# Optimization experiments

Measured on AMD Instinct MI355X. Metric: run time of the kernel, lower is better.

The kernel has to match this reference:

```python
import jax, jax.numpy as jnp
import numpy as np

K = 1024       # num_embeddings
D = 64         # embedding_dim
DECAY = 0.99
COMMIT = 0.25
EPS = 1e-05


def setup_inputs() -> dict:
    key = jax.random.key(0)
    k1, k2, k3 = jax.random.split(key, 3)
    x = jax.random.normal(k1, (16, 64, 64, 64), jnp.float32)  # NCHW, C == D
    embedding_weight = jax.random.normal(k2, (K, D), jnp.float32)
    ema_weight = jax.random.normal(k3, (K, D), jnp.float32)
    ema_cluster_size = jnp.zeros((K,), jnp.float32)
    return {"x": x, "embedding_weight": embedding_weight,
            "ema_cluster_size": ema_cluster_size, "ema_weight": ema_weight}


def reference(x, embedding_weight, ema_cluster_size, ema_weight):
    # NCHW -> NHWC, flatten tokens
    xp = jnp.transpose(x, (0, 2, 3, 1))            # [B,H,W,D]
    flat = xp.reshape(-1, D)                        # [N,D]
    dists = ((flat ** 2).sum(1, keepdims=True)
             + (embedding_weight ** 2).sum(1)
             - 2.0 * flat @ embedding_weight.T)     # [N,K]
    idx = jnp.argmin(dists, axis=1)                 # [N]
    encodings = jax.nn.one_hot(idx, K, dtype=flat.dtype)  # [N,K]
    quantized = jnp.take(embedding_weight, idx, axis=0).reshape(xp.shape)
    # training-mode EMA updates (scatter-add instead of dense one-hot matmuls)
    counts = jnp.zeros((K,), flat.dtype).at[idx].add(1.0)
    new_cs = ema_cluster_size * DECAY + (1.0 - DECAY) * counts
    n = new_cs.sum()
    new_cs = (new_cs + EPS) / (n + K * EPS) * n     # Laplace smoothing
    dw = jnp.zeros((K, D), flat.dtype).at[idx].add(flat)
    new_ema_weight = ema_weight * DECAY + (1.0 - DECAY) * dw
    new_embedding = new_ema_weight / new_cs[:, None]
    # commitment loss and straight-through estimator
    e_latent_loss = jnp.mean((jax.lax.stop_gradient(quantized) - xp) ** 2)
    loss = COMMIT * e_latent_loss
    q_st = xp + jax.lax.stop_gradient(quantized - xp)
    return (loss, jnp.transpose(q_st, (0, 3, 1, 2)), encodings,
            new_embedding, new_cs, new_ema_weight)
```

## Files before the change

kernel.cpp:

```cpp
#include <hip/hip_runtime.h>

#define HW 4096
#define DECAYF 0.99f
#define ONEMF 0.01f
#define EPSF 1e-5f

typedef __bf16 bf16x8 __attribute__((ext_vector_type(8)));
typedef float f32x4 __attribute__((ext_vector_type(4)));
typedef unsigned short ushort8 __attribute__((ext_vector_type(8)));

#define WS_COUNTS 65536
#define WS_NCHALF 66560
#define WS_SSE    67584
#define WS_EHI    67600
#define WS_ELO    100368

__device__ __forceinline__ float wave_reduce_add(float v) {
#pragma unroll
    for (int o = 32; o > 0; o >>= 1) v += __shfl_xor(v, o, 64);
    return v;
}

__device__ __forceinline__ unsigned short bf_rne(float f) {
    unsigned int u = __float_as_uint(f);
    unsigned int r = u + 0x7fffu + ((u >> 16) & 1u);
    return (unsigned short)(r >> 16);
}

__global__ __launch_bounds__(256) void prep_kernel(const float* __restrict__ E,
                                                   float* __restrict__ ws) {
    const int bid = blockIdx.x, tid = threadIdx.x;
    const int id = bid * 256 + tid;
    ws[id] = 0.0f;
    if (bid < 4) ws[WS_COUNTS + bid * 256 + tid] = 0.0f;
    if (bid == 4 && tid == 0) ws[WS_SSE] = 0.0f;
    const float v = E[id];
    const unsigned short h = bf_rne(v);
    const float hf = __uint_as_float((unsigned int)h << 16);
    const unsigned short l = bf_rne(v - hf);
    ((unsigned short*)(ws + WS_EHI))[id] = h;
    ((unsigned short*)(ws + WS_ELO))[id] = l;
    const int lane = tid & 63;
    const float s = wave_reduce_add(v * v);
    if (lane == 0) ws[WS_NCHALF + (id >> 6)] = -0.5f * s;
}

__global__ __launch_bounds__(256) void vq_main(const float* __restrict__ x,
                                               const float* __restrict__ E,
                                               float* __restrict__ out,
                                               float* __restrict__ ws) {
    const int tid = threadIdx.x;
    const int lane = tid & 63;
    const int w = tid >> 6;
    const int blk = blockIdx.x;
    const int b = blk >> 5;
    const int hw0 = (blk & 31) << 7;
    const int tok0 = blk << 7;

    __shared__ float xs[128 * 68];
    __shared__ int i1sh[128], i2sh[128], idx_sh[128];

    {
        const float* xb = x + ((size_t)b << 18) + hw0;
#pragma unroll
        for (int cc = 0; cc < 32; ++cc) {
            const int id = cc * 256 + tid;
            const int c = id >> 7, t = id & 127;
            xs[t * 68 + c] = xb[((size_t)c << 12) + t];
        }
    }
    __syncthreads();

    const int q = lane >> 4, m = lane & 15;

    bf16x8 Ah[2][2], Al[2][2];
#pragma unroll
    for (int t = 0; t < 2; ++t) {
        const int tok = w * 32 + t * 16 + m;
#pragma unroll
        for (int s = 0; s < 2; ++s) {
            const float* p = &xs[tok * 68 + s * 32 + q * 8];
            ushort8 hu, lu;
#pragma unroll
            for (int j = 0; j < 8; ++j) {
                const float f = p[j];
                const unsigned short h = bf_rne(f);
                const float hf = __uint_as_float((unsigned int)h << 16);
                hu[j] = h;
                lu[j] = bf_rne(f - hf);
            }
            Ah[t][s] = __builtin_bit_cast(bf16x8, hu);
            Al[t][s] = __builtin_bit_cast(bf16x8, lu);
        }
    }

    const ushort8* __restrict__ Ehp = (const ushort8*)(ws + WS_EHI);
    const ushort8* __restrict__ Elp = (const ushort8*)(ws + WS_ELO);
    const float* __restrict__ ncp = ws + WS_NCHALF;

    float b1[2][4], b2[2][4];
    int i1[2][4], i2[2][4];
#pragma unroll
    for (int t = 0; t < 2; ++t)
#pragma unroll
        for (int r = 0; r < 4; ++r) { b1[t][r] = -1e30f; b2[t][r] = -1e30f; i1[t][r] = 0; i2[t][r] = 1; }

    ushort8 nb0h = Ehp[m * 8 + q];
    ushort8 nb1h = Ehp[m * 8 + 4 + q];
    ushort8 nb0l = Elp[m * 8 + q];
    ushort8 nb1l = Elp[m * 8 + 4 + q];
    float nnc = ncp[m];

    for (int ck = 0; ck < 64; ++ck) {
        const ushort8 c0h = nb0h, c1h = nb1h, c0l = nb0l, c1l = nb1l;
        const float nc = nnc;
        if (ck < 63) {
            const int code = (ck + 1) * 16 + m;
            nb0h = Ehp[code * 8 + q];
            nb1h = Ehp[code * 8 + 4 + q];
            nb0l = Elp[code * 8 + q];
            nb1l = Elp[code * 8 + 4 + q];
            nnc = ncp[code];
        }
        const bf16x8 bh0 = __builtin_bit_cast(bf16x8, c0h);
        const bf16x8 bh1 = __builtin_bit_cast(bf16x8, c1h);
        const bf16x8 bl0 = __builtin_bit_cast(bf16x8, c0l);
        const bf16x8 bl1 = __builtin_bit_cast(bf16x8, c1l);
        const int idx = ck * 16 + m;
#pragma unroll
        for (int t = 0; t < 2; ++t) {
            f32x4 acc = {nc, nc, nc, nc};
            acc = __builtin_amdgcn_mfma_f32_16x16x32_bf16(Ah[t][0], bh0, acc, 0, 0, 0);
            acc = __builtin_amdgcn_mfma_f32_16x16x32_bf16(Ah[t][1], bh1, acc, 0, 0, 0);
            acc = __builtin_amdgcn_mfma_f32_16x16x32_bf16(Al[t][0], bh0, acc, 0, 0, 0);
            acc = __builtin_amdgcn_mfma_f32_16x16x32_bf16(Al[t][1], bh1, acc, 0, 0, 0);
            acc = __builtin_amdgcn_mfma_f32_16x16x32_bf16(Ah[t][0], bl0, acc, 0, 0, 0);
            acc = __builtin_amdgcn_mfma_f32_16x16x32_bf16(Ah[t][1], bl1, acc, 0, 0, 0);
#pragma unroll
            for (int r = 0; r < 4; ++r) {
                const float s = acc[r];
                const bool cA = s > b1[t][r];
                const bool cB = s > b2[t][r];
                b2[t][r] = cA ? b1[t][r] : (cB ? s : b2[t][r]);
                i2[t][r] = cA ? i1[t][r] : (cB ? idx : i2[t][r]);
                b1[t][r] = cA ? s : b1[t][r];
                i1[t][r] = cA ? idx : i1[t][r];
            }
        }
    }

#pragma unroll
    for (int d = 1; d < 16; d <<= 1) {
#pragma unroll
        for (int t = 0; t < 2; ++t)
#pragma unroll
            for (int r = 0; r < 4; ++r) {
                const float ob1 = __shfl_xor(b1[t][r], d, 64);
                const int   oi1 = __shfl_xor(i1[t][r], d, 64);
                const float ob2 = __shfl_xor(b2[t][r], d, 64);
                const int   oi2 = __shfl_xor(i2[t][r], d, 64);
                const bool wv = ob1 > b1[t][r];
                const float t1 = wv ? ob1 : b1[t][r]; const int ti1 = wv ? oi1 : i1[t][r];
                const float sA = wv ? b1[t][r] : ob1; const int siA = wv ? i1[t][r] : oi1;
                const float sB = wv ? ob2 : b2[t][r]; const int siB = wv ? oi2 : i2[t][r];
                const bool w2 = sB > sA;
                b1[t][r] = t1; i1[t][r] = ti1;
                b2[t][r] = w2 ? sB : sA; i2[t][r] = w2 ? siB : siA;
            }
    }
    if (m == 0) {
#pragma unroll
        for (int t = 0; t < 2; ++t)
#pragma unroll
            for (int r = 0; r < 4; ++r) {
                const int tokL = w * 32 + t * 16 + q * 4 + r;
                i1sh[tokL] = i1[t][r];
                i2sh[tokL] = i2[t][r];
            }
    }

    float dval = 0.0f;
    if (lane < 32) {
        const int tokL = w * 32 + lane;
        const int I1 = i1sh[tokL], I2 = i2sh[tokL];
        const int ca = I1 < I2 ? I1 : I2;
        const int cb = I1 < I2 ? I2 : I1;
        const float* Ea = E + ca * 64;
        const float* Eb = E + cb * 64;
        const float* xr = &xs[tokL * 68];
        double sa = 0, ea = 0, sb = 0, eb = 0, x2 = 0;
#pragma unroll 8
        for (int c = 0; c < 64; ++c) {
            const double xv = (double)xr[c];
            const double va = (double)Ea[c], vb = (double)Eb[c];
            sa += xv * va; ea += va * va;
            sb += xv * vb; eb += vb * vb;
            x2 += xv * xv;
        }
        const double qa = ea - 2.0 * sa;
        const double qb = eb - 2.0 * sb;
        int best; double qq;
        if (qb < qa) { best = cb; qq = qb; } else { best = ca; qq = qa; }
        idx_sh[tokL] = best;
        float dd = (float)(qq + x2);
        dval = dd < 0.f ? 0.f : dd;
        atomicAdd(&ws[WS_COUNTS + best], 1.0f);
    }
    const float ssum = wave_reduce_add(dval);
    if (lane == 0) atomicAdd(&ws[WS_SSE], ssum);
    __syncthreads();

    float* outq = out + 1;
#pragma unroll
    for (int cc = 0; cc < 32; ++cc) {
        const int id = cc * 256 + tid;
        const int c = id >> 7, t = id & 127;
        const int kb = idx_sh[t];
        const float xv = xs[t * 68 + c];
        const float eq = E[kb * 64 + c];
        outq[((size_t)(b * 64 + c) << 12) + hw0 + t] = xv + (eq - xv);
    }
#pragma unroll 4
    for (int tt = 0; tt < 32; ++tt) {
        const int t = w * 32 + tt;
        const int kb = idx_sh[t];
        atomicAdd(&ws[kb * 64 + lane], xs[t * 68 + lane]);
    }
    {
        float* enc = out + 1 + (size_t)4194304;
        const int c0 = tid << 2;
        for (int t = 0; t < 128; ++t) {
            const int kb = idx_sh[t];
            f32x4 v;
            v[0] = (c0 == kb) ? 1.0f : 0.0f;
            v[1] = (c0 + 1 == kb) ? 1.0f : 0.0f;
            v[2] = (c0 + 2 == kb) ? 1.0f : 0.0f;
            v[3] = (c0 + 3 == kb) ? 1.0f : 0.0f;
            __builtin_nontemporal_store(v, (f32x4*)(enc + (size_t)(tok0 + t) * 1024 + c0));
        }
    }
}

__global__ __launch_bounds__(1024) void fin_cs(const float* __restrict__ cs_in,
                                               float* __restrict__ out,
                                               const float* __restrict__ ws) {
    __shared__ float red[16];
    __shared__ float n_sh;
    const int tid = threadIdx.x;
    const float raw = cs_in[tid] * DECAYF + ONEMF * ws[WS_COUNTS + tid];
    const float s = wave_reduce_add(raw);
    if ((tid & 63) == 0) red[tid >> 6] = s;
    __syncthreads();
    if (tid == 0) {
        float n = 0.f;
#pragma unroll
        for (int i = 0; i < 16; ++i) n += red[i];
        n_sh = n;
        out[0] = 0.25f * ws[WS_SSE] * (1.0f / 4194304.0f);
    }
    __syncthreads();
    const float n = n_sh;
    out[71368705 + tid] = (raw + EPSF) / (n + 1024.0f * EPSF) * n;
}

__global__ __launch_bounds__(256) void fin_w(const float* __restrict__ emaw,
                                             float* __restrict__ out,
                                             const float* __restrict__ ws) {
    const int i = blockIdx.x * 256 + threadIdx.x;
    const float val = emaw[i] * DECAYF + ONEMF * ws[i];
    out[71369729 + i] = val;
    const float cs = out[71368705 + (i >> 6)];
    out[71303169 + i] = val / cs;
}

extern "C" void kernel_launch(void* const* d_in, const int* in_sizes, int n_in,
                              void* d_out, int out_size, void* d_ws, size_t ws_size,
                              hipStream_t stream) {
    const float* x    = (const float*)d_in[0];
    const float* E    = (const float*)d_in[1];
    const float* cs   = (const float*)d_in[2];
    const float* emaw = (const float*)d_in[3];
    float* out = (float*)d_out;
    float* ws  = (float*)d_ws;

    prep_kernel<<<256, 256, 0, stream>>>(E, ws);
    vq_main<<<512, 256, 0, stream>>>(x, E, out, ws);
    fin_cs<<<1, 1024, 0, stream>>>(cs, out, ws);
    fin_w<<<256, 256, 0, stream>>>(emaw, out, ws);
}
```

Baseline: 418.9 us.

## Split VQ kernel into scoring and output-writing kernels with double-buffered codebook prefetch

The fused kernel is split in two. vq_score computes the nearest-code indices and writes them to workspace. vq_out runs on 2048 blocks of 32 tokens and writes the quantized output, the one-hot encodings and the dw scatter-adds. The scoring loop now prefetches the codebook two steps ahead in alternating register slots instead of one. The aim is to spread the heavy encoding-write traffic (16M floats) over more blocks for better memory parallelism, and to hide codebook load latency. The cost is an extra launch, re-reading x, and an index round-trip through global memory.

```diff
diff --git a/kernel.cpp b/kernel.cpp
--- a/kernel.cpp
+++ b/kernel.cpp
@@ -1,6 +1,5 @@
 #include <hip/hip_runtime.h>
 
-#define HW 4096
 #define DECAYF 0.99f
 #define ONEMF 0.01f
 #define EPSF 1e-5f
@@ -14,6 +13,7 @@
 #define WS_SSE    67584
 #define WS_EHI    67600
 #define WS_ELO    100368
+#define WS_IDX    133136
 
 __device__ __forceinline__ float wave_reduce_add(float v) {
 #pragma unroll
@@ -45,10 +45,9 @@
     if (lane == 0) ws[WS_NCHALF + (id >> 6)] = -0.5f * s;
 }
 
-__global__ __launch_bounds__(256) void vq_main(const float* __restrict__ x,
-                                               const float* __restrict__ E,
-                                               float* __restrict__ out,
-                                               float* __restrict__ ws) {
+__global__ __launch_bounds__(256) void vq_score(const float* __restrict__ x,
+                                                const float* __restrict__ E,
+                                                float* __restrict__ ws) {
     const int tid = threadIdx.x;
     const int lane = tid & 63;
     const int w = tid >> 6;
@@ -58,7 +57,7 @@
     const int tok0 = blk << 7;
 
     __shared__ float xs[128 * 68];
-    __shared__ int i1sh[128], i2sh[128], idx_sh[128];
+    __shared__ int i1sh[128], i2sh[128];
 
     {
         const float* xb = x + ((size_t)b << 18) + hw0;
@@ -105,49 +104,61 @@
 #pragma unroll
         for (int r = 0; r < 4; ++r) { b1[t][r] = -1e30f; b2[t][r] = -1e30f; i1[t][r] = 0; i2[t][r] = 1; }
 
-    ushort8 nb0h = Ehp[m * 8 + q];
-    ushort8 nb1h = Ehp[m * 8 + 4 + q];
-    ushort8 nb0l = Elp[m * 8 + q];
-    ushort8 nb1l = Elp[m * 8 + 4 + q];
-    float nnc = ncp[m];
-
-    for (int ck = 0; ck < 64; ++ck) {
-        const ushort8 c0h = nb0h, c1h = nb1h, c0l = nb0l, c1l = nb1l;
-        const float nc = nnc;
-        if (ck < 63) {
-            const int code = (ck + 1) * 16 + m;
-            nb0h = Ehp[code * 8 + q];
-            nb1h = Ehp[code * 8 + 4 + q];
-            nb0l = Elp[code * 8 + q];
-            nb1l = Elp[code * 8 + 4 + q];
-            nnc = ncp[code];
-        }
-        const bf16x8 bh0 = __builtin_bit_cast(bf16x8, c0h);
-        const bf16x8 bh1 = __builtin_bit_cast(bf16x8, c1h);
-        const bf16x8 bl0 = __builtin_bit_cast(bf16x8, c0l);
-        const bf16x8 bl1 = __builtin_bit_cast(bf16x8, c1l);
-        const int idx = ck * 16 + m;
-#pragma unroll
-        for (int t = 0; t < 2; ++t) {
-            f32x4 acc = {nc, nc, nc, nc};
-            acc = __builtin_amdgcn_mfma_f32_16x16x32_bf16(Ah[t][0], bh0, acc, 0, 0, 0);
-            acc = __builtin_amdgcn_mfma_f32_16x16x32_bf16(Ah[t][1], bh1, acc, 0, 0, 0);
-            acc = __builtin_amdgcn_mfma_f32_16x16x32_bf16(Al[t][0], bh0, acc, 0, 0, 0);
-            acc = __builtin_amdgcn_mfma_f32_16x16x32_bf16(Al[t][1], bh1, acc, 0, 0, 0);
-            acc = __builtin_amdgcn_mfma_f32_16x16x32_bf16(Ah[t][0], bl0, acc, 0, 0, 0);
-            acc = __builtin_amdgcn_mfma_f32_16x16x32_bf16(Ah[t][1], bl1, acc, 0, 0, 0);
-#pragma unroll
-            for (int r = 0; r < 4; ++r) {
-                const float s = acc[r];
-                const bool cA = s > b1[t][r];
-                const bool cB = s > b2[t][r];
-                b2[t][r] = cA ? b1[t][r] : (cB ? s : b2[t][r]);
-                i2[t][r] = cA ? i1[t][r] : (cB ? idx : i2[t][r]);
-                b1[t][r] = cA ? s : b1[t][r];
-                i1[t][r] = cA ? idx : i1[t][r];
-            }
-        }
-    }
+    ushort8 p0h[2], p1h[2], p0l[2], p1l[2];
+    float pnc[2];
+#pragma unroll
+    for (int s = 0; s < 2; ++s) {
+        const int code = s * 16 + m;
+        p0h[s] = Ehp[code * 8 + q];
+        p1h[s] = Ehp[code * 8 + 4 + q];
+        p0l[s] = Elp[code * 8 + q];
+        p1l[s] = Elp[code * 8 + 4 + q];
+        pnc[s] = ncp[code];
+    }
+
+#define VQ_STEP(S, CK)                                                          \
+    {                                                                           \
+        const bf16x8 bh0 = __builtin_bit_cast(bf16x8, p0h[S]);                  \
+        const bf16x8 bh1 = __builtin_bit_cast(bf16x8, p1h[S]);                  \
+        const bf16x8 bl0 = __builtin_bit_cast(bf16x8, p0l[S]);                  \
+        const bf16x8 bl1 = __builtin_bit_cast(bf16x8, p1l[S]);                  \
+        const float nc = pnc[S];                                                \
+        if ((CK) + 2 < 64) {                                                    \
+            const int code = ((CK) + 2) * 16 + m;                               \
+            p0h[S] = Ehp[code * 8 + q];                                         \
+            p1h[S] = Ehp[code * 8 + 4 + q];                                     \
+            p0l[S] = Elp[code * 8 + q];                                         \
+            p1l[S] = Elp[code * 8 + 4 + q];                                     \
+            pnc[S] = ncp[code];                                                 \
+        }                                                                       \
+        const int idx = (CK) * 16 + m;                                          \
+        _Pragma("unroll")                                                       \
+        for (int t = 0; t < 2; ++t) {                                           \
+            f32x4 acc = {nc, nc, nc, nc};         \
+            acc = __builtin_amdgcn_mfma_f32_16x16x32_bf16(Ah[t][0], bh0, acc, 0, 0, 0); \
+            acc = __builtin_amdgcn_mfma_f32_16x16x32_bf16(Ah[t][1], bh1, acc, 0, 0, 0); \
+            acc = __builtin_amdgcn_mfma_f32_16x16x32_bf16(Al[t][0], bh0, acc, 0, 0, 0); \
+            acc = __builtin_amdgcn_mfma_f32_16x16x32_bf16(Al[t][1], bh1, acc, 0, 0, 0); \
+            acc = __builtin_amdgcn_mfma_f32_16x16x32_bf16(Ah[t][0], bl0, acc, 0, 0, 0); \
+            acc = __builtin_amdgcn_mfma_f32_16x16x32_bf16(Ah[t][1], bl1, acc, 0, 0, 0); \
+            _Pragma("unroll")                                                   \
+            for (int r = 0; r < 4; ++r) {                                       \
+                const float s = acc[r];                                         \
+                const bool cA = s > b1[t][r];                                   \
+                const bool cB = s > b2[t][r];                                   \
+                b2[t][r] = cA ? b1[t][r] : (cB ? s : b2[t][r]);                 \
+                i2[t][r] = cA ? i1[t][r] : (cB ? idx : i2[t][r]);               \
+                b1[t][r] = cA ? s : b1[t][r];                                   \
+                i1[t][r] = cA ? idx : i1[t][r];                                 \
+            }                                                                   \
+        }                                                                       \
+    }
+
+    for (int j = 0; j < 32; ++j) {
+        VQ_STEP(0, 2 * j)
+        VQ_STEP(1, 2 * j + 1)
+    }
+#undef VQ_STEP
 
 #pragma unroll
     for (int d = 1; d < 16; d <<= 1) {
@@ -201,36 +212,64 @@
         const double qb = eb - 2.0 * sb;
         int best; double qq;
         if (qb < qa) { best = cb; qq = qb; } else { best = ca; qq = qa; }
-        idx_sh[tokL] = best;
+        ((int*)(ws + WS_IDX))[tok0 + tokL] = best;
         float dd = (float)(qq + x2);
         dval = dd < 0.f ? 0.f : dd;
         atomicAdd(&ws[WS_COUNTS + best], 1.0f);
     }
     const float ssum = wave_reduce_add(dval);
     if (lane == 0) atomicAdd(&ws[WS_SSE], ssum);
+}
+
+__global__ __launch_bounds__(256) void vq_out(const float* __restrict__ x,
+                                              const float* __restrict__ E,
+                                              float* __restrict__ out,
+                                              float* __restrict__ ws) {
+    const int tid = threadIdx.x;
+    const int lane = tid & 63;
+    const int w = tid >> 6;
+    const int blk = blockIdx.x;
+    const int b = blk >> 7;
+    const int hw0 = (blk & 127) << 5;
+    const int tok0 = blk << 5;
+
+    __shared__ float xsb[32 * 65];
+    __shared__ float eqb[32 * 65];
+    __shared__ int idxb[32];
+
+    if (tid < 32) idxb[tid] = ((const int*)(ws + WS_IDX))[tok0 + tid];
+    {
+        const float* xb = x + ((size_t)b << 18) + hw0;
+#pragma unroll
+        for (int cc = 0; cc < 8; ++cc) {
+            const int id = cc * 256 + tid;
+            const int t = id & 31, c = id >> 5;
+            xsb[t * 65 + c] = xb[((size_t)c << 12) + t];
+        }
+    }
+    __syncthreads();
+#pragma unroll
+    for (int j = 0; j < 8; ++j) {
+        const int t = w * 8 + j;
+        eqb[t * 65 + lane] = E[idxb[t] * 64 + lane];
+    }
     __syncthreads();
 
     float* outq = out + 1;
 #pragma unroll
-    for (int cc = 0; cc < 32; ++cc) {
-        const int id = cc * 256 + tid;
-        const int c = id >> 7, t = id & 127;
-        const int kb = idx_sh[t];
-        const float xv = xs[t * 68 + c];
-        const float eq = E[kb * 64 + c];
+    for (int cc = 0; cc < 8; ++cc) {
+        const int c = cc * 8 + (tid >> 5);
+        const int t = tid & 31;
+        const float xv = xsb[t * 65 + c];
+        const float eq = eqb[t * 65 + c];
         outq[((size_t)(b * 64 + c) << 12) + hw0 + t] = xv + (eq - xv);
     }
-#pragma unroll 4
-    for (int tt = 0; tt < 32; ++tt) {
-        const int t = w * 32 + tt;
-        const int kb = idx_sh[t];
-        atomicAdd(&ws[kb * 64 + lane], xs[t * 68 + lane]);
-    }
+
     {
         float* enc = out + 1 + (size_t)4194304;
         const int c0 = tid << 2;
-        for (int t = 0; t < 128; ++t) {
-            const int kb = idx_sh[t];
+        for (int t = 0; t < 32; ++t) {
+            const int kb = idxb[t];
             f32x4 v;
             v[0] = (c0 == kb) ? 1.0f : 0.0f;
             v[1] = (c0 + 1 == kb) ? 1.0f : 0.0f;
@@ -238,6 +277,13 @@
             v[3] = (c0 + 3 == kb) ? 1.0f : 0.0f;
             __builtin_nontemporal_store(v, (f32x4*)(enc + (size_t)(tok0 + t) * 1024 + c0));
         }
+    }
+
+#pragma unroll
+    for (int j = 0; j < 8; ++j) {
+        const int t = w * 8 + j;
+        const int kb = idxb[t];
+        atomicAdd(&ws[kb * 64 + lane], xsb[t * 65 + lane]);
     }
 }
 
@@ -284,7 +330,8 @@
     float* ws  = (float*)d_ws;
 
     prep_kernel<<<256, 256, 0, stream>>>(E, ws);
-    vq_main<<<512, 256, 0, stream>>>(x, E, out, ws);
+    vq_score<<<512, 256, 0, stream>>>(x, E, ws);
+    vq_out<<<2048, 256, 0, stream>>>(x, E, out, ws);
     fin_cs<<<1, 1024, 0, stream>>>(cs, out, ws);
     fin_w<<<256, 256, 0, stream>>>(emaw, out, ws);
 }
```

Result: no change. 422.1 us (+0.7%).
